# Kernel tuning notes

Measured on AMD Instinct MI355X. Metric: run time of the kernel, lower is better.

## Reference

```python
import jax, jax.numpy as jnp
import numpy as np

B, D_IN, H, D_OUT = 1024, 512, 512, 512


def _act(v):
    # torch.relu(x) ** 2
    r = jnp.maximum(v, 0.0)
    return r * r


def setup_inputs() -> dict:
    key = jax.random.key(0)
    ks = jax.random.split(key, 8)
    x = jax.random.normal(ks[0], (B, D_IN), dtype=jnp.float32)
    # input_to_hidden: Linear(D_IN, H)
    W_in = jax.random.normal(ks[1], (D_IN, H), dtype=jnp.float32) / np.sqrt(D_IN)
    b_in = jax.random.normal(ks[2], (H,), dtype=jnp.float32) * 0.01
    # hidden_to_hidden[i]: Linear(1, H-i-1). Pack into padded arrays [H-1, H]
    # where row i, column j is the weight feeding output index j (valid only j > i).
    W_hh = jax.random.normal(ks[3], (H - 1, H), dtype=jnp.float32) * 0.02
    b_hh = jax.random.normal(ks[4], (H - 1, H), dtype=jnp.float32) * 0.01
    # hidden_to_output: Linear(H, D_OUT)
    W_out = jax.random.normal(ks[5], (H, D_OUT), dtype=jnp.float32) / np.sqrt(H)
    b_out = jax.random.normal(ks[6], (D_OUT,), dtype=jnp.float32) * 0.01
    return {"x": x, "W_in": W_in, "b_in": b_in, "W_hh": W_hh, "b_hh": b_hh,
            "W_out": W_out, "b_out": b_out}


def reference(x, W_in, b_in, W_hh, b_hh, W_out, b_out):
    h0 = _act(x @ W_in + b_in)  # [B, H]
    hid = h0.shape[1]
    col = jnp.arange(hid)

    def step(h, inp):
        i, w, b = inp  # w, b: [H] padded rows
        src = jnp.take(h, i, axis=1)  # [B], uses UPDATED h (strict sequential dep)
        contrib = _act(src[:, None] * w[None, :] + b[None, :])  # [B, H]
        mask = (col > i).astype(h.dtype)  # only columns i+1.. get updated
        return h + contrib * mask[None, :], None

    xs = (jnp.arange(hid - 1), W_hh, b_hh)
    h, _ = jax.lax.scan(step, h0, xs)
    return h @ W_out + b_out  # [B, D_OUT]
```

## Files before the change

kernel.cpp:

```cpp
#include <hip/hip_runtime.h>

#define B_SZ 1024
#define DIN 512
#define HH 512
#define DOUT 512

typedef short bf16x8 __attribute__((ext_vector_type(8)));
typedef float f32x4 __attribute__((ext_vector_type(4)));

__device__ __forceinline__ unsigned short f2bf(float f) {
    unsigned int u = __float_as_uint(f);
    u += 0x7FFFu + ((u >> 16) & 1u);
    return (unsigned short)(u >> 16);
}
__device__ __forceinline__ float bf2f(unsigned short s) {
    return __uint_as_float(((unsigned int)s) << 16);
}

__device__ __forceinline__ void conv_split_body(const float* __restrict__ src,
                                                uint4* __restrict__ dst, int t) {
    const int lane = t & 63;
    const int fb   = t >> 6;
    const int ks   = fb >> 6;
    const int mf   = fb & 63;
    const int row  = mf * 16 + (lane & 15);
    const int kb   = ks * 32 + ((lane >> 4) << 3);
    const int term = kb >> 9;
    const int c    = kb & 511;
    const float4 a0 = *(const float4*)&src[(size_t)row * 512 + c];
    const float4 a1 = *(const float4*)&src[(size_t)row * 512 + c + 4];
    const float av[8] = {a0.x, a0.y, a0.z, a0.w, a1.x, a1.y, a1.z, a1.w};
    unsigned short o[8];
    #pragma unroll
    for (int j = 0; j < 8; ++j) {
        unsigned short hi = f2bf(av[j]);
        o[j] = (term == 1) ? f2bf(av[j] - bf2f(hi)) : hi;
    }
    uint4 v;
    v.x = (unsigned int)o[0] | ((unsigned int)o[1] << 16);
    v.y = (unsigned int)o[2] | ((unsigned int)o[3] << 16);
    v.z = (unsigned int)o[4] | ((unsigned int)o[5] << 16);
    v.w = (unsigned int)o[6] | ((unsigned int)o[7] << 16);
    dst[t] = v;
}

__device__ __forceinline__ void convW_body(const float* __restrict__ W,
                                           uint4* __restrict__ dst, int t) {
    const int lane = t & 63;
    const int fb   = t >> 6;
    const int ks   = fb >> 5;
    const int nf   = fb & 31;
    const int col  = nf * 16 + (lane & 15);
    const int kb   = ks * 32 + ((lane >> 4) << 3);
    const int term = kb >> 9;
    const int c0   = kb & 511;
    unsigned short o[8];
    #pragma unroll
    for (int j = 0; j < 8; ++j) {
        const float f = W[(size_t)(c0 + j) * 512 + col];
        unsigned short hi = f2bf(f);
        o[j] = (term == 2) ? f2bf(f - bf2f(hi)) : hi;
    }
    uint4 v;
    v.x = (unsigned int)o[0] | ((unsigned int)o[1] << 16);
    v.y = (unsigned int)o[2] | ((unsigned int)o[3] << 16);
    v.z = (unsigned int)o[4] | ((unsigned int)o[5] << 16);
    v.w = (unsigned int)o[6] | ((unsigned int)o[7] << 16);
    dst[t] = v;
}

__global__ __launch_bounds__(256)
void prep_all(const float* __restrict__ W_hh, const float* __restrict__ b_hh,
              float2* __restrict__ wb,
              const float* __restrict__ x, uint4* __restrict__ Afr,
              const float* __restrict__ W_in, uint4* __restrict__ Bin,
              const float* __restrict__ W_out, uint4* __restrict__ Bout) {
    const int b = blockIdx.x;
    const int tid = threadIdx.x;
    if (b < 1022) {
        const int idx = b * 256 + tid;
        const int i = idx >> 9;
        const int j = idx & 511;
        float2 o;
        if (j > i) { o.x = W_hh[idx]; o.y = b_hh[idx]; }
        else       { o.x = 0.0f;      o.y = -1.0f;     }
        wb[idx] = o;
    } else if (b < 1790) {
        conv_split_body(x, Afr, (b - 1022) * 256 + tid);
    } else if (b < 2174) {
        convW_body(W_in, Bin, (b - 1790) * 256 + tid);
    } else {
        convW_body(W_out, Bout, (b - 2174) * 256 + tid);
    }
}

__global__ __launch_bounds__(256)
void conv_h(const float* __restrict__ h, uint4* __restrict__ Afr) {
    conv_split_body(h, Afr, blockIdx.x * 256 + threadIdx.x);
}

template <bool ACT>
__global__ __launch_bounds__(256)
void mfma_gemm(const uint4* __restrict__ Ag,
               const uint4* __restrict__ Bg,
               const float* __restrict__ bias,
               float* __restrict__ C) {
    __shared__ uint4 lds[2][768];
    const int tid  = threadIdx.x;
    const int lane = tid & 63;
    const int w    = tid >> 6;
    const int wr   = w & 1;
    const int wc   = w >> 1;
    const int mf0  = blockIdx.x * 4;
    const int nf0  = blockIdx.y * 2;

    const int a_mfs = (tid >> 6) & 3;
    const int b_ks  = tid >> 7;
    const int b_nfs = (tid >> 6) & 1;

    uint4 R0, R1, R2;
    auto stage = [&](int s) {
        const int ks0 = s * 2;
        R0 = Ag[(size_t)((ks0    ) * 64 + mf0 + a_mfs) * 64 + lane];
        R1 = Ag[(size_t)((ks0 + 1) * 64 + mf0 + a_mfs) * 64 + lane];
        R2 = Bg[(size_t)((ks0 + b_ks) * 32 + nf0 + b_nfs) * 64 + lane];
    };

    f32x4 acc0 = {0.f, 0.f, 0.f, 0.f};
    f32x4 acc1 = {0.f, 0.f, 0.f, 0.f};

    stage(0);
    lds[0][tid] = R0; lds[0][256 + tid] = R1; lds[0][512 + tid] = R2;
    stage(1);
    __syncthreads();

    for (int s = 0; s < 24; ++s) {
        const int cur = s & 1;
        if (s + 1 < 24) {
            const int nxt = cur ^ 1;
            lds[nxt][tid] = R0; lds[nxt][256 + tid] = R1; lds[nxt][512 + tid] = R2;
        }
        if (s + 2 < 24) stage(s + 2);
        __builtin_amdgcn_sched_barrier(0);

        bf16x8 aF[2][2], bF[2];
        #pragma unroll
        for (int ksL = 0; ksL < 2; ++ksL) {
            #pragma unroll
            for (int mfL = 0; mfL < 2; ++mfL)
                aF[ksL][mfL] = *(const bf16x8*)&lds[cur][ksL * 256 + (wr * 2 + mfL) * 64 + lane];
            bF[ksL] = *(const bf16x8*)&lds[cur][512 + (ksL * 2 + wc) * 64 + lane];
        }
        #pragma unroll
        for (int ksL = 0; ksL < 2; ++ksL) {
            acc0 = __builtin_amdgcn_mfma_f32_16x16x32_bf16(aF[ksL][0], bF[ksL], acc0, 0, 0, 0);
            acc1 = __builtin_amdgcn_mfma_f32_16x16x32_bf16(aF[ksL][1], bF[ksL], acc1, 0, 0, 0);
        }
        __syncthreads();
    }

    const int colg   = (nf0 + wc) * 16 + (lane & 15);
    const float bv   = bias[colg];
    const int rbase0 = (mf0 + wr * 2) * 16 + ((lane >> 4) << 2);
    #pragma unroll
    for (int r = 0; r < 4; ++r) {
        float v = acc0[r] + bv;
        if (ACT) { v = fmaxf(v, 0.f); v = v * v; }
        C[(size_t)(rbase0 + r) * 512 + colg] = v;
    }
    #pragma unroll
    for (int r = 0; r < 4; ++r) {
        float v = acc1[r] + bv;
        if (ACT) { v = fmaxf(v, 0.f); v = v * v; }
        C[(size_t)(rbase0 + 16 + r) * 512 + colg] = v;
    }
}

template <int C>
__device__ __forceinline__ void scan_chunk(const float2* __restrict__ wb,
                                           float hr[8], int lane) {
    constexpr int NK = 8 - C;
    constexpr int PF = (C < 4) ? 4 : (C < 6) ? 8 : 16;
    constexpr int NT = 64 / PF;
    const float2* base = wb + (size_t)(64 * C) * HH + 64 * C + lane;

    float2 Wb[PF][NK];
    #pragma unroll
    for (int q = 0; q < PF; ++q)
        #pragma unroll
        for (int k = 0; k < NK; ++k)
            Wb[q][k] = base[(size_t)q * HH + 64 * k];

    for (int t = 0; t < NT; ++t) {
        #pragma unroll
        for (int q = 0; q < PF; ++q) {
            const int s = t * PF + q;
            const float hi = __uint_as_float(
                __builtin_amdgcn_readlane(__float_as_uint(hr[C]), s));
            if (C != 7 || s != 63) {
                #pragma unroll
                for (int k = 0; k < NK; ++k) {
                    const float tv = fmaf(hi, Wb[q][k].x, Wb[q][k].y);
                    const float rv = fmaxf(tv, 0.f);
                    hr[C + k] = fmaf(rv, rv, hr[C + k]);
                }
            }
            if (t + 1 < NT) {
                #pragma unroll
                for (int k = 0; k < NK; ++k)
                    Wb[q][k] = base[(size_t)(s + PF) * HH + 64 * k];
            }
        }
    }
}

__global__ __launch_bounds__(256)
void scan_kernel(const float2* __restrict__ wb, float* __restrict__ h) {
    const int lane = threadIdx.x & 63;
    const int wave = threadIdx.x >> 6;
    const int row  = blockIdx.x * 4 + wave;
    float* hrow = h + (size_t)row * HH;

    float hr[8];
    #pragma unroll
    for (int k = 0; k < 8; ++k) hr[k] = hrow[lane + 64 * k];

    scan_chunk<0>(wb, hr, lane);
    scan_chunk<1>(wb, hr, lane);
    scan_chunk<2>(wb, hr, lane);
    scan_chunk<3>(wb, hr, lane);
    scan_chunk<4>(wb, hr, lane);
    scan_chunk<5>(wb, hr, lane);
    scan_chunk<6>(wb, hr, lane);
    scan_chunk<7>(wb, hr, lane);

    #pragma unroll
    for (int k = 0; k < 8; ++k) hrow[lane + 64 * k] = hr[k];
}

extern "C" void kernel_launch(void* const* d_in, const int* in_sizes, int n_in,
                              void* d_out, int out_size, void* d_ws, size_t ws_size,
                              hipStream_t stream) {
    const float* x     = (const float*)d_in[0];
    const float* W_in  = (const float*)d_in[1];
    const float* b_in  = (const float*)d_in[2];
    const float* W_hh  = (const float*)d_in[3];
    const float* b_hh  = (const float*)d_in[4];
    const float* W_out = (const float*)d_in[5];
    const float* b_out = (const float*)d_in[6];
    float* out = (float*)d_out;

    char* ws = (char*)d_ws;
    float2* wb  = (float2*)ws;
    float*  h   = (float*)(ws + 0x200000u);
    uint4*  Afr = (uint4*)(ws + 0x400000u);
    uint4*  Bin = (uint4*)(ws + 0x700000u);
    uint4*  Bout= (uint4*)(ws + 0x880000u);

    prep_all<<<dim3(2558), dim3(256), 0, stream>>>(W_hh, b_hh, wb,
                                                   x, Afr, W_in, Bin, W_out, Bout);

    mfma_gemm<true><<<dim3(16, 16), dim3(256), 0, stream>>>(Afr, Bin, b_in, h);

    scan_kernel<<<dim3(256), dim3(256), 0, stream>>>(wb, h);

    conv_h<<<dim3(768), dim3(256), 0, stream>>>(h, Afr);

    mfma_gemm<false><<<dim3(16, 16), dim3(256), 0, stream>>>(Afr, Bout, b_out, out);
}
```

Measured before the change: 157.4 us.

## Fuse activation bf16 split into GEMM loads and restructure scan chunk loads

The GEMM now reads fp32 activations directly and converts them to split bf16 hi/lo fragments while staging into LDS. This removes the separate conv_h kernel and the x conversion pass, along with their global round trips. The scan kernel is also restructured: each chunk first preloads all 64 diagonal-block weights and processes the sequential diagonal column alone, then updates the remaining columns with deeper prefetch. Launch bounds are set to one block per SM, and a __syncthreads is added per chunk. The trade-off is that the fp32 loads and conversion ALU now sit inside the GEMM loop, and register pressure in the scan rises.

```diff
diff --git a/kernel.cpp b/kernel.cpp
--- a/kernel.cpp
+++ b/kernel.cpp
@@ -15,33 +15,6 @@
 }
 __device__ __forceinline__ float bf2f(unsigned short s) {
     return __uint_as_float(((unsigned int)s) << 16);
-}
-
-__device__ __forceinline__ void conv_split_body(const float* __restrict__ src,
-                                                uint4* __restrict__ dst, int t) {
-    const int lane = t & 63;
-    const int fb   = t >> 6;
-    const int ks   = fb >> 6;
-    const int mf   = fb & 63;
-    const int row  = mf * 16 + (lane & 15);
-    const int kb   = ks * 32 + ((lane >> 4) << 3);
-    const int term = kb >> 9;
-    const int c    = kb & 511;
-    const float4 a0 = *(const float4*)&src[(size_t)row * 512 + c];
-    const float4 a1 = *(const float4*)&src[(size_t)row * 512 + c + 4];
-    const float av[8] = {a0.x, a0.y, a0.z, a0.w, a1.x, a1.y, a1.z, a1.w};
-    unsigned short o[8];
-    #pragma unroll
-    for (int j = 0; j < 8; ++j) {
-        unsigned short hi = f2bf(av[j]);
-        o[j] = (term == 1) ? f2bf(av[j] - bf2f(hi)) : hi;
-    }
-    uint4 v;
-    v.x = (unsigned int)o[0] | ((unsigned int)o[1] << 16);
-    v.y = (unsigned int)o[2] | ((unsigned int)o[3] << 16);
-    v.z = (unsigned int)o[4] | ((unsigned int)o[5] << 16);
-    v.w = (unsigned int)o[6] | ((unsigned int)o[7] << 16);
-    dst[t] = v;
 }
 
 __device__ __forceinline__ void convW_body(const float* __restrict__ W,
@@ -72,7 +45,6 @@
 __global__ __launch_bounds__(256)
 void prep_all(const float* __restrict__ W_hh, const float* __restrict__ b_hh,
               float2* __restrict__ wb,
-              const float* __restrict__ x, uint4* __restrict__ Afr,
               const float* __restrict__ W_in, uint4* __restrict__ Bin,
               const float* __restrict__ W_out, uint4* __restrict__ Bout) {
     const int b = blockIdx.x;
@@ -85,23 +57,16 @@
         if (j > i) { o.x = W_hh[idx]; o.y = b_hh[idx]; }
         else       { o.x = 0.0f;      o.y = -1.0f;     }
         wb[idx] = o;
-    } else if (b < 1790) {
-        conv_split_body(x, Afr, (b - 1022) * 256 + tid);
-    } else if (b < 2174) {
-        convW_body(W_in, Bin, (b - 1790) * 256 + tid);
+    } else if (b < 1406) {
+        convW_body(W_in, Bin, (b - 1022) * 256 + tid);
     } else {
-        convW_body(W_out, Bout, (b - 2174) * 256 + tid);
-    }
-}
-
-__global__ __launch_bounds__(256)
-void conv_h(const float* __restrict__ h, uint4* __restrict__ Afr) {
-    conv_split_body(h, Afr, blockIdx.x * 256 + threadIdx.x);
+        convW_body(W_out, Bout, (b - 1406) * 256 + tid);
+    }
 }
 
 template <bool ACT>
-__global__ __launch_bounds__(256)
-void mfma_gemm(const uint4* __restrict__ Ag,
+__global__ __launch_bounds__(256, 1)
+void mfma_gemm(const float* __restrict__ A,
                const uint4* __restrict__ Bg,
                const float* __restrict__ bias,
                float* __restrict__ C) {
@@ -118,28 +83,56 @@
     const int b_ks  = tid >> 7;
     const int b_nfs = (tid >> 6) & 1;
 
-    uint4 R0, R1, R2;
+    const int arow = (mf0 + a_mfs) * 16 + (lane & 15);
+    const int koff = (lane >> 4) << 3;
+
+    float4 Ra0, Ra1, Rb0, Rb1;
+    uint4  R2;
     auto stage = [&](int s) {
         const int ks0 = s * 2;
-        R0 = Ag[(size_t)((ks0    ) * 64 + mf0 + a_mfs) * 64 + lane];
-        R1 = Ag[(size_t)((ks0 + 1) * 64 + mf0 + a_mfs) * 64 + lane];
-        R2 = Bg[(size_t)((ks0 + b_ks) * 32 + nf0 + b_nfs) * 64 + lane];
+        const int c0 = (ks0 * 32 + koff) & 511;
+        const int c1 = ((ks0 + 1) * 32 + koff) & 511;
+        Ra0 = *(const float4*)&A[(size_t)arow * 512 + c0];
+        Ra1 = *(const float4*)&A[(size_t)arow * 512 + c0 + 4];
+        Rb0 = *(const float4*)&A[(size_t)arow * 512 + c1];
+        Rb1 = *(const float4*)&A[(size_t)arow * 512 + c1 + 4];
+        R2  = Bg[(size_t)((ks0 + b_ks) * 32 + nf0 + b_nfs) * 64 + lane];
+    };
+
+    auto cvt8 = [&](const float4& a0, const float4& a1, int term) -> uint4 {
+        const float av[8] = {a0.x, a0.y, a0.z, a0.w, a1.x, a1.y, a1.z, a1.w};
+        unsigned int p[4];
+        #pragma unroll
+        for (int q = 0; q < 4; ++q) {
+            float f0 = av[2 * q], f1 = av[2 * q + 1];
+            unsigned short h0 = f2bf(f0), h1 = f2bf(f1);
+            if (term == 1) {
+                h0 = f2bf(f0 - bf2f(h0));
+                h1 = f2bf(f1 - bf2f(h1));
+            }
+            p[q] = (unsigned int)h0 | ((unsigned int)h1 << 16);
+        }
+        uint4 v; v.x = p[0]; v.y = p[1]; v.z = p[2]; v.w = p[3];
+        return v;
+    };
+    auto write_tile = [&](int buf, int s) {
+        const int ks0 = s * 2;
+        lds[buf][tid]       = cvt8(Ra0, Ra1, ks0 >> 4);
+        lds[buf][256 + tid] = cvt8(Rb0, Rb1, (ks0 + 1) >> 4);
+        lds[buf][512 + tid] = R2;
     };
 
     f32x4 acc0 = {0.f, 0.f, 0.f, 0.f};
     f32x4 acc1 = {0.f, 0.f, 0.f, 0.f};
 
     stage(0);
-    lds[0][tid] = R0; lds[0][256 + tid] = R1; lds[0][512 + tid] = R2;
+    write_tile(0, 0);
     stage(1);
     __syncthreads();
 
     for (int s = 0; s < 24; ++s) {
         const int cur = s & 1;
-        if (s + 1 < 24) {
-            const int nxt = cur ^ 1;
-            lds[nxt][tid] = R0; lds[nxt][256 + tid] = R1; lds[nxt][512 + tid] = R2;
-        }
+        if (s + 1 < 24) write_tile(cur ^ 1, s + 1);
         if (s + 2 < 24) stage(s + 2);
         __builtin_amdgcn_sched_barrier(0);
 
@@ -179,42 +172,65 @@
 template <int C>
 __device__ __forceinline__ void scan_chunk(const float2* __restrict__ wb,
                                            float hr[8], int lane) {
-    constexpr int NK = 8 - C;
-    constexpr int PF = (C < 4) ? 4 : (C < 6) ? 8 : 16;
-    constexpr int NT = 64 / PF;
-    const float2* base = wb + (size_t)(64 * C) * HH + 64 * C + lane;
-
-    float2 Wb[PF][NK];
-    #pragma unroll
-    for (int q = 0; q < PF; ++q)
-        #pragma unroll
-        for (int k = 0; k < NK; ++k)
-            Wb[q][k] = base[(size_t)q * HH + 64 * k];
-
-    for (int t = 0; t < NT; ++t) {
-        #pragma unroll
-        for (int q = 0; q < PF; ++q) {
-            const int s = t * PF + q;
+    constexpr int NK = 7 - C;
+    constexpr int D  = (NK >= 4) ? 8 : (NK >= 2) ? 16 : 32;
+    const float2* rowp = wb + (size_t)(64 * C) * HH + lane;
+
+    __syncthreads();
+
+    float2 Wd[64];
+    #pragma unroll
+    for (int s = 0; s < 64; ++s)
+        Wd[s] = rowp[(size_t)s * HH + 64 * C];
+
+    float2 Wb[NK > 0 ? D : 1][NK > 0 ? NK : 1];
+    if constexpr (NK > 0) {
+        #pragma unroll
+        for (int q = 0; q < D; ++q)
+            #pragma unroll
+            for (int k = 0; k < NK; ++k)
+                Wb[q][k] = rowp[(size_t)q * HH + 64 * (C + 1 + k)];
+    }
+    asm volatile("s_waitcnt vmcnt(0)");
+    __builtin_amdgcn_sched_barrier(0);
+
+    #pragma unroll
+    for (int s = 0; s < 64; ++s) {
+        if (!(C == 7 && s == 63)) {
             const float hi = __uint_as_float(
                 __builtin_amdgcn_readlane(__float_as_uint(hr[C]), s));
-            if (C != 7 || s != 63) {
+            const float tv = fmaf(hi, Wd[s].x, Wd[s].y);
+            const float rv = fmaxf(tv, 0.f);
+            hr[C] = fmaf(rv, rv, hr[C]);
+        }
+    }
+
+    if constexpr (NK > 0) {
+        constexpr int NT = 64 / D;
+        for (int t = 0; t < NT; ++t) {
+            #pragma unroll
+            for (int q = 0; q < D; ++q) {
+                const int i = t * D + q;
+                const float hi = __uint_as_float(
+                    __builtin_amdgcn_readlane(__float_as_uint(hr[C]), i));
                 #pragma unroll
                 for (int k = 0; k < NK; ++k) {
                     const float tv = fmaf(hi, Wb[q][k].x, Wb[q][k].y);
                     const float rv = fmaxf(tv, 0.f);
-                    hr[C + k] = fmaf(rv, rv, hr[C + k]);
+                    hr[C + 1 + k] = fmaf(rv, rv, hr[C + 1 + k]);
+                }
+                if (t + 1 < NT) {
+                    #pragma unroll
+                    for (int k = 0; k < NK; ++k)
+                        Wb[q][k] = rowp[(size_t)(i + D) * HH + 64 * (C + 1 + k)];
                 }
             }
-            if (t + 1 < NT) {
-                #pragma unroll
-                for (int k = 0; k < NK; ++k)
-                    Wb[q][k] = base[(size_t)(s + PF) * HH + 64 * k];
-            }
-        }
-    }
-}
-
-__global__ __launch_bounds__(256)
+            __builtin_amdgcn_sched_barrier(0);
+        }
+    }
+}
+
+__global__ __launch_bounds__(256, 1)
 void scan_kernel(const float2* __restrict__ wb, float* __restrict__ h) {
     const int lane = threadIdx.x & 63;
     const int wave = threadIdx.x >> 6;
@@ -251,20 +267,17 @@
     float* out = (float*)d_out;
 
     char* ws = (char*)d_ws;
-    float2* wb  = (float2*)ws;
-    float*  h   = (float*)(ws + 0x200000u);
-    uint4*  Afr = (uint4*)(ws + 0x400000u);
-    uint4*  Bin = (uint4*)(ws + 0x700000u);
-    uint4*  Bout= (uint4*)(ws + 0x880000u);
-
-    prep_all<<<dim3(2558), dim3(256), 0, stream>>>(W_hh, b_hh, wb,
-                                                   x, Afr, W_in, Bin, W_out, Bout);
-
-    mfma_gemm<true><<<dim3(16, 16), dim3(256), 0, stream>>>(Afr, Bin, b_in, h);
+    float2* wb   = (float2*)ws;
+    float*  h    = (float*)(ws + 0x200000u);
+    uint4*  Bin  = (uint4*)(ws + 0x400000u);
+    uint4*  Bout = (uint4*)(ws + 0x580000u);
+
+    prep_all<<<dim3(1790), dim3(256), 0, stream>>>(W_hh, b_hh, wb,
+                                                   W_in, Bin, W_out, Bout);
+
+    mfma_gemm<true><<<dim3(16, 16), dim3(256), 0, stream>>>(x, Bin, b_in, h);
 
     scan_kernel<<<dim3(256), dim3(256), 0, stream>>>(wb, h);
 
-    conv_h<<<dim3(768), dim3(256), 0, stream>>>(h, Afr);
-
-    mfma_gemm<false><<<dim3(16, 16), dim3(256), 0, stream>>>(Afr, Bout, b_out, out);
-}
+    mfma_gemm<false><<<dim3(16, 16), dim3(256), 0, stream>>>(h, Bout, b_out, out);
+}
```

New measurement: 218.6 us. 38.8% more time.
